# Kernel optimization log

Hardware: AMD Instinct MI355X
Metric: run time of the kernel (lower is better)

## Reference

```python
import jax, jax.numpy as jnp
import numpy as np

TOPK = 9
NUM_CLASSES = 80
IMG = 640
STRIDES = (8, 16, 32)
EPS_IOU = 1e-6   # mmdet BboxOverlaps2D union clamp
EPS_GT = 1e-9    # select_candidates_in_gts eps


def _make_anchors():
    boxes, levels = [], []
    for s in STRIDES:
        n = IMG // s
        c = (np.arange(n, dtype=np.float32) + 0.5) * s
        cx, cy = np.meshgrid(c, c)
        ctr = np.stack([cx.ravel(), cy.ravel()], -1)
        half = 2.5 * s
        boxes.append(np.concatenate([ctr - half, ctr + half], -1))
        levels.append(n * n)
    return np.concatenate(boxes, 0).astype(np.float32), np.array(levels, np.int64)


def setup_inputs() -> dict:
    key = jax.random.key(0)
    ks = jax.random.split(key, 6)
    bs, n_max = 32, 64
    anc, levels = _make_anchors()
    A = anc.shape[0]
    xy = jax.random.uniform(ks[0], (bs, n_max, 2)) * 560.0
    wh = jax.random.uniform(ks[1], (bs, n_max, 2)) * 120.0 + 8.0
    gt_bboxes = jnp.concatenate([xy, xy + wh], -1)
    pxy = jax.random.uniform(ks[2], (bs, A, 2)) * 560.0
    pwh = jax.random.uniform(ks[3], (bs, A, 2)) * 120.0 + 8.0
    pd_bboxes = jnp.concatenate([pxy, pxy + pwh], -1)
    gt_labels = jax.random.randint(ks[4], (bs, n_max, 1), 0, NUM_CLASSES)
    mask_gt = (jax.random.uniform(ks[5], (bs, n_max, 1)) < 0.8).astype(jnp.float32)
    return {"anc_bboxes": jnp.asarray(anc), "n_level_bboxes": levels,
            "gt_labels": gt_labels, "gt_bboxes": gt_bboxes,
            "mask_gt": mask_gt, "pd_bboxes": pd_bboxes}


def _assign(anc_bboxes, levels, gt_labels, gt_bboxes, mask_gt, pd_bboxes):
    A = anc_bboxes.shape[0]
    bs, n_max, _ = gt_bboxes.shape
    gt_flat = gt_bboxes.reshape(-1, 4)
    # pairwise IoU gt vs anchors (mmdet BboxOverlaps2D), (bs, n_max, A)
    lt = jnp.maximum(gt_flat[:, None, :2], anc_bboxes[None, :, :2])
    rb = jnp.minimum(gt_flat[:, None, 2:], anc_bboxes[None, :, 2:])
    inter = jnp.clip(rb - lt, 0).prod(-1)
    area_g = jnp.clip(gt_flat[:, 2:] - gt_flat[:, :2], 0).prod(-1)
    area_a = jnp.clip(anc_bboxes[:, 2:] - anc_bboxes[:, :2], 0).prod(-1)
    union = jnp.maximum(area_g[:, None] + area_a[None, :] - inter, EPS_IOU)
    overlaps = (inter / union).reshape(bs, n_max, A)
    # center distances, (bs, n_max, A)
    gt_c = (gt_flat[:, :2] + gt_flat[:, 2:]) * 0.5
    ac_c = (anc_bboxes[:, :2] + anc_bboxes[:, 2:]) * 0.5
    dist = jnp.sqrt(((gt_c[:, None, :] - ac_c[None, :, :]) ** 2).sum(-1)).reshape(bs, n_max, A)
    # per-level topk (smallest distance) candidates
    mask_gt_b = mask_gt > 0  # (bs, n_max, 1)
    row = jnp.arange(bs * n_max)[:, None]
    is_in_list, idx_list = [], []
    start = 0
    for L in levels:
        k = min(TOPK, L)
        d = dist[..., start:start + L]
        _, idxs = jax.lax.top_k(-d, k)  # (bs, n_max, k)
        idx_list.append(idxs + start)
        idxs_m = jnp.where(mask_gt_b, idxs, 0).reshape(bs * n_max, k)
        cnt = jnp.zeros((bs * n_max, L), dist.dtype).at[row, idxs_m].add(1.0)
        cnt = cnt.reshape(bs, n_max, L)
        is_in_list.append(jnp.where(cnt > 1, jnp.zeros_like(cnt), cnt))
        start += L
    is_in_candidate = jnp.concatenate(is_in_list, -1)  # (bs, n_max, A)
    candidate_idxs = jnp.concatenate(idx_list, -1)     # (bs, n_max, n_levels*k)
    # ATSS threshold = mean + std (unbiased) over candidate overlaps
    cand_ov_full = jnp.where(is_in_candidate > 0, overlaps, jnp.zeros_like(overlaps))
    cand = jnp.take_along_axis(cand_ov_full.reshape(bs * n_max, A),
                               candidate_idxs.reshape(bs * n_max, -1), axis=1)
    cand = cand.reshape(bs, n_max, -1)
    thr = cand.mean(-1, keepdims=True) + cand.std(-1, keepdims=True, ddof=1)
    is_pos = jnp.where(cand_ov_full > thr, is_in_candidate, jnp.zeros_like(is_in_candidate))
    # anchor centers strictly inside gt boxes
    deltas = jnp.concatenate([ac_c[None, None] - gt_bboxes[:, :, None, :2],
                              gt_bboxes[:, :, None, 2:] - ac_c[None, None]], -1)
    is_in_gts = (deltas.min(-1) > EPS_GT).astype(dist.dtype)
    mask_pos = is_pos * is_in_gts * mask_gt  # (bs, n_max, A)
    # resolve anchors assigned to multiple gts by highest IoU (always applied; no-op if no conflicts)
    fg_mask = mask_pos.sum(1)  # (bs, A)
    multi = fg_mask[:, None, :] > 1
    is_max = jnp.transpose(jax.nn.one_hot(overlaps.argmax(1), n_max, dtype=overlaps.dtype), (0, 2, 1))
    mask_pos = jnp.where(multi, is_max, mask_pos)
    fg_mask = mask_pos.sum(1)
    target_gt_idx = mask_pos.argmax(1)  # (bs, A)
    # gather targets
    flat_idx = (target_gt_idx + jnp.arange(bs)[:, None] * n_max).reshape(-1)
    target_labels = gt_labels.reshape(-1)[flat_idx].reshape(bs, A)
    target_labels = jnp.where(fg_mask > 0, target_labels, NUM_CLASSES)
    target_bboxes = gt_flat[flat_idx].reshape(bs, A, 4)
    target_scores = jax.nn.one_hot(target_labels, NUM_CLASSES + 1, dtype=overlaps.dtype)[..., :NUM_CLASSES]
    # scale scores by IoU(gt, pred) of the assigned gt
    lt2 = jnp.maximum(gt_bboxes[:, :, None, :2], pd_bboxes[:, None, :, :2])
    rb2 = jnp.minimum(gt_bboxes[:, :, None, 2:], pd_bboxes[:, None, :, 2:])
    ov2 = jnp.clip(rb2 - lt2, 0).prod(-1)
    a1 = jnp.clip(gt_bboxes[:, :, 2:] - gt_bboxes[:, :, :2], 0).prod(-1)[:, :, None]
    a2 = jnp.clip(pd_bboxes[:, :, 2:] - pd_bboxes[:, :, :2], 0).prod(-1)[:, None, :]
    ious = ov2 / (a1 + a2 - ov2 + 1e-9) * mask_pos
    target_scores = target_scores * jnp.max(ious, axis=1)[..., None]
    return target_labels.astype(jnp.int32), target_bboxes, target_scores, fg_mask > 0


def reference(anc_bboxes, n_level_bboxes, gt_labels, gt_bboxes, mask_gt, pd_bboxes):
    levels = [int(v) for v in np.asarray(n_level_bboxes)]
    return _assign(anc_bboxes, levels, gt_labels, gt_bboxes, mask_gt, pd_bboxes)
```

## Files before the change

### kernel.cpp

```cpp
#include <hip/hip_runtime.h>
#include <stdint.h>

#pragma clang fp contract(off)

#define BS 32
#define NMAX 64
#define A_TOT 8400
#define NC 80

template<int N, int S, int START, int C0>
__device__ __forceinline__ void select_and_iou(
    int ilo, int jlo, float gcx, float gcy,
    float x1, float y1, float x2, float y2, float area_g,
    float* __restrict__ ovrow, int* __restrict__ idxrow)
{
  unsigned long long kk[9];
#pragma unroll
  for (int i = 0; i < 9; ++i) kk[i] = ~0ULL;
  const float s = (float)S;
#pragma unroll
  for (int di = 0; di < 5; ++di) {
    int ii = ilo + di;
    float ay = ((float)ii + 0.5f) * s;
    float dy = gcy - ay;
    float dy2 = dy * dy;
#pragma unroll
    for (int dj = 0; dj < 5; ++dj) {
      int jj = jlo + dj;
      float ax = ((float)jj + 0.5f) * s;
      float dx = gcx - ax;
      float d = sqrtf(dx * dx + dy2);
      unsigned long long key =
          ((unsigned long long)__float_as_uint(d) << 32) |
          (unsigned int)(START + ii * N + jj);
      if (key < kk[8]) {
        kk[8] = key;
#pragma unroll
        for (int t = 8; t > 0; --t) {
          unsigned long long lo = kk[t], hi = kk[t - 1];
          if (lo < hi) { kk[t] = hi; kk[t - 1] = lo; }
        }
      }
    }
  }
#pragma unroll
  for (int t = 0; t < 9; ++t) {
    int aa = (int)(kk[t] & 0xffffffffULL);
    int loc = aa - START;
    int ii = loc / N;
    int jj = loc - ii * N;
    float cx = ((float)jj + 0.5f) * s;
    float cy = ((float)ii + 0.5f) * s;
    const float h = 2.5f * (float)S;
    float ax1 = cx - h, ay1 = cy - h, ax2 = cx + h, ay2 = cy + h;
    float iw = fminf(x2, ax2) - fmaxf(x1, ax1); iw = fmaxf(iw, 0.f);
    float ih = fminf(y2, ay2) - fmaxf(y1, ay1); ih = fmaxf(ih, 0.f);
    float inter = iw * ih;
    float area_a = fmaxf(ax2 - ax1, 0.f) * fmaxf(ay2 - ay1, 0.f);
    float uni = fmaxf(area_g + area_a - inter, 1e-6f);
    ovrow[C0 + t] = inter / uni;
    idxrow[C0 + t] = aa;
  }
}

template<int N, int S, int START, int C0>
__device__ __forceinline__ void scatter_level(
    const float* __restrict__ ovrow, const int* __restrict__ idxrow,
    float thr, float x1, float y1, float x2, float y2,
    int a0, int na, int g, int* s_cnt, int* s_gmin)
{
  const float s = (float)S;
#pragma unroll
  for (int t = 0; t < 9; ++t) {
    float o = ovrow[C0 + t];
    if (o > thr) {
      int aa = idxrow[C0 + t];
      if (aa >= a0 && aa < a0 + na) {
        int loc = aa - START;
        int ii = loc / N;
        int jj = loc - ii * N;
        float cx = ((float)jj + 0.5f) * s;
        float cy = ((float)ii + 0.5f) * s;
        float m = fminf(fminf(cx - x1, cy - y1), fminf(x2 - cx, y2 - cy));
        if (m > 1e-9f) {
          atomicAdd(&s_cnt[aa - a0], 1);
          atomicMin(&s_gmin[aa - a0], g);
        }
      }
    }
  }
}


__global__ __launch_bounds__(256) void atss_fused_k(
    const int* __restrict__ gt_labels,
    const float* __restrict__ gt_bboxes,
    const float* __restrict__ mask_gt,
    const float* __restrict__ pd_bboxes,
    float* __restrict__ out)
{
  __shared__ float s_gt[NMAX * 4];
  __shared__ int   s_lab[NMAX];
  __shared__ float s_ov[NMAX][27];
  __shared__ int   s_idx[NMAX][27];
  __shared__ int   s_cnt[256];
  __shared__ int   s_gmin[256];
  __shared__ int   s_alab[256];
  __shared__ float s_asc[256];

  const int b   = blockIdx.y;
  const int a0  = blockIdx.x * 256;
  const int na  = min(256, A_TOT - a0);
  const int tid = threadIdx.x;

  s_gt[tid] = gt_bboxes[(size_t)b * NMAX * 4 + tid];
  if (tid < NMAX) s_lab[tid] = gt_labels[b * NMAX + tid];
  s_cnt[tid]  = 0;
  s_gmin[tid] = NMAX;
  __syncthreads();

  if (tid < NMAX) {
    const int g = tid;
    if (mask_gt[b * NMAX + g] > 0.0f) {
      float x1 = s_gt[g * 4 + 0], y1 = s_gt[g * 4 + 1];
      float x2 = s_gt[g * 4 + 2], y2 = s_gt[g * 4 + 3];
      float gcx = (x1 + x2) * 0.5f;
      float gcy = (y1 + y2) * 0.5f;

      int jlo0 = min(max((int)floorf(gcx / 8.f)  - 2, 0), 80 - 5);
      int ilo0 = min(max((int)floorf(gcy / 8.f)  - 2, 0), 80 - 5);
      int jlo1 = min(max((int)floorf(gcx / 16.f) - 2, 0), 40 - 5);
      int ilo1 = min(max((int)floorf(gcy / 16.f) - 2, 0), 40 - 5);
      int jlo2 = min(max((int)floorf(gcx / 32.f) - 2, 0), 20 - 5);
      int ilo2 = min(max((int)floorf(gcy / 32.f) - 2, 0), 20 - 5);

      int lo0 = ilo0 * 80 + jlo0,          hi0 = (ilo0 + 4) * 80 + jlo0 + 4;
      int lo1 = 6400 + ilo1 * 40 + jlo1,   hi1 = 6400 + (ilo1 + 4) * 40 + jlo1 + 4;
      int lo2 = 8000 + ilo2 * 20 + jlo2,   hi2 = 8000 + (ilo2 + 4) * 20 + jlo2 + 4;
      bool act = (lo0 < a0 + na && hi0 >= a0) ||
                 (lo1 < a0 + na && hi1 >= a0) ||
                 (lo2 < a0 + na && hi2 >= a0);

      if (act) {
        float area_g = fmaxf(x2 - x1, 0.f) * fmaxf(y2 - y1, 0.f);
        float* ovrow = s_ov[g];
        int*   idxrow = s_idx[g];
        select_and_iou<80,  8,    0,  0>(ilo0, jlo0, gcx, gcy, x1, y1, x2, y2, area_g, ovrow, idxrow);
        select_and_iou<40, 16, 6400,  9>(ilo1, jlo1, gcx, gcy, x1, y1, x2, y2, area_g, ovrow, idxrow);
        select_and_iou<20, 32, 8000, 18>(ilo2, jlo2, gcx, gcy, x1, y1, x2, y2, area_g, ovrow, idxrow);

        float sum = 0.f;
#pragma unroll
        for (int c = 0; c < 27; ++c) sum += ovrow[c];
        float mean = sum / 27.f;
        float ss = 0.f;
#pragma unroll
        for (int c = 0; c < 27; ++c) { float d = ovrow[c] - mean; ss += d * d; }
        float thr = mean + sqrtf(ss / 26.f);

        scatter_level<80,  8,    0,  0>(ovrow, idxrow, thr, x1, y1, x2, y2, a0, na, g, s_cnt, s_gmin);
        scatter_level<40, 16, 6400,  9>(ovrow, idxrow, thr, x1, y1, x2, y2, a0, na, g, s_cnt, s_gmin);
        scatter_level<20, 32, 8000, 18>(ovrow, idxrow, thr, x1, y1, x2, y2, a0, na, g, s_cnt, s_gmin);
      }
    }
  }
  __syncthreads();

  const int a = a0 + tid;
  int lab = NC; float sc = 0.f; int gsel = 0; int fg = 0;

  if (a < A_TOT) {
    const size_t ia = (size_t)b * A_TOT + a;
    const float4 pb = *(const float4*)(pd_bboxes + ia * 4);
    const int c = s_cnt[tid];
    if (c == 1) { gsel = s_gmin[tid]; fg = 1; }
    else if (c > 1) {
      float cx, cy, h;
      if (a < 6400)      { int ii = a / 80;          int jj = a - ii * 80;  cx = ((float)jj + 0.5f) * 8.f;  cy = ((float)ii + 0.5f) * 8.f;  h = 20.f; }
      else if (a < 8000) { int loc = a - 6400; int ii = loc / 40; int jj = loc - ii * 40; cx = ((float)jj + 0.5f) * 16.f; cy = ((float)ii + 0.5f) * 16.f; h = 40.f; }
      else               { int loc = a - 8000; int ii = loc / 20; int jj = loc - ii * 20; cx = ((float)jj + 0.5f) * 32.f; cy = ((float)ii + 0.5f) * 32.f; h = 80.f; }
      float ax1 = cx - h, ay1 = cy - h, ax2 = cx + h, ay2 = cy + h;
      float area_a = fmaxf(ax2 - ax1, 0.f) * fmaxf(ay2 - ay1, 0.f);
      float best = -1.f; int bg = 0;
      for (int gg = 0; gg < NMAX; ++gg) {
        float x1 = s_gt[gg * 4 + 0], y1 = s_gt[gg * 4 + 1];
        float x2 = s_gt[gg * 4 + 2], y2 = s_gt[gg * 4 + 3];
        float iw = fminf(x2, ax2) - fmaxf(x1, ax1); iw = fmaxf(iw, 0.f);
        float ih = fminf(y2, ay2) - fmaxf(y1, ay1); ih = fmaxf(ih, 0.f);
        float inter = iw * ih;
        float ag = fmaxf(x2 - x1, 0.f) * fmaxf(y2 - y1, 0.f);
        float uni = fmaxf(ag + area_a - inter, 1e-6f);
        float iou = inter / uni;
        if (iou > best) { best = iou; bg = gg; }
      }
      gsel = bg; fg = 1;
    }

    if (fg) {
      lab = s_lab[gsel];
      float x1 = s_gt[gsel * 4 + 0], y1 = s_gt[gsel * 4 + 1];
      float x2 = s_gt[gsel * 4 + 2], y2 = s_gt[gsel * 4 + 3];
      float iw = fminf(x2, pb.z) - fmaxf(x1, pb.x); iw = fmaxf(iw, 0.f);
      float ih = fminf(y2, pb.w) - fmaxf(y1, pb.y); ih = fmaxf(ih, 0.f);
      float inter = iw * ih;
      float ag = fmaxf(x2 - x1, 0.f) * fmaxf(y2 - y1, 0.f);
      float ap = fmaxf(pb.z - pb.x, 0.f) * fmaxf(pb.w - pb.y, 0.f);
      sc = inter / (ag + ap - inter + 1e-9f);
    }

    out[ia] = (float)lab;
    float4 bb = { s_gt[gsel * 4 + 0], s_gt[gsel * 4 + 1],
                  s_gt[gsel * 4 + 2], s_gt[gsel * 4 + 3] };
    *(float4*)(out + (size_t)BS * A_TOT + ia * 4) = bb;
    out[(size_t)BS * A_TOT * 85 + ia] = fg ? 1.0f : 0.0f;
  }

  s_alab[tid] = lab;
  s_asc[tid]  = sc;
  __syncthreads();

  float* outS = out + (size_t)BS * A_TOT * 5 + ((size_t)b * A_TOT + a0) * NC;
  const int nv4 = na * (NC / 4);
  for (int i = tid; i < nv4; i += 256) {
    int al = i / (NC / 4);
    int c4 = (i - al * (NC / 4)) * 4;
    int L  = s_alab[al];
    float sv = s_asc[al];
    float4 v;
    v.x = (L == c4 + 0) ? sv : 0.f;
    v.y = (L == c4 + 1) ? sv : 0.f;
    v.z = (L == c4 + 2) ? sv : 0.f;
    v.w = (L == c4 + 3) ? sv : 0.f;
    ((float4*)outS)[i] = v;
  }
}


extern "C" void kernel_launch(void* const* d_in, const int* in_sizes, int n_in,
                              void* d_out, int out_size, void* d_ws, size_t ws_size,
                              hipStream_t stream) {
  const int*   gt_labels = (const int*)  d_in[2];
  const float* gt_bboxes = (const float*)d_in[3];
  const float* mask_gt   = (const float*)d_in[4];
  const float* pd_bboxes = (const float*)d_in[5];
  float* out = (float*)d_out;

  atss_fused_k<<<dim3((A_TOT + 255) / 256, BS), 256, 0, stream>>>(
      gt_labels, gt_bboxes, mask_gt, pd_bboxes, out);
}
```

Before: 136.9 us.

## Split per-GT level top-k across 192 threads and use nontemporal output stores

The serial per-GT candidate selection over three pyramid levels, previously done by 64 threads, is split so that 192 threads each handle one (GT, level) pair. Window bounds and an active flag are staged in shared memory, and two extra barriers separate the phases. Separately, all output writes now use nontemporal stores, so the large score tensor writes stream past the cache. The aim is to shorten the latency-bound selection phase and reduce cache pollution, at the cost of extra synchronisation and shared memory traffic.

```diff
diff --git a/kernel.cpp b/kernel.cpp
--- a/kernel.cpp
+++ b/kernel.cpp
@@ -7,6 +7,8 @@
 #define NMAX 64
 #define A_TOT 8400
 #define NC 80
+
+typedef float vfloat4 __attribute__((ext_vector_type(4)));
 
 template<int N, int S, int START, int C0>
 __device__ __forceinline__ void select_and_iou(
@@ -107,6 +109,9 @@
   __shared__ int   s_gmin[256];
   __shared__ int   s_alab[256];
   __shared__ float s_asc[256];
+  __shared__ short s_ilo[3][NMAX];
+  __shared__ short s_jlo[3][NMAX];
+  __shared__ unsigned char s_act[NMAX];
 
   const int b   = blockIdx.y;
   const int a0  = blockIdx.x * 256;
@@ -121,6 +126,7 @@
 
   if (tid < NMAX) {
     const int g = tid;
+    bool act = false;
     if (mask_gt[b * NMAX + g] > 0.0f) {
       float x1 = s_gt[g * 4 + 0], y1 = s_gt[g * 4 + 1];
       float x2 = s_gt[g * 4 + 2], y2 = s_gt[g * 4 + 3];
@@ -133,36 +139,62 @@
       int ilo1 = min(max((int)floorf(gcy / 16.f) - 2, 0), 40 - 5);
       int jlo2 = min(max((int)floorf(gcx / 32.f) - 2, 0), 20 - 5);
       int ilo2 = min(max((int)floorf(gcy / 32.f) - 2, 0), 20 - 5);
+      s_jlo[0][g] = (short)jlo0; s_ilo[0][g] = (short)ilo0;
+      s_jlo[1][g] = (short)jlo1; s_ilo[1][g] = (short)ilo1;
+      s_jlo[2][g] = (short)jlo2; s_ilo[2][g] = (short)ilo2;
 
       int lo0 = ilo0 * 80 + jlo0,          hi0 = (ilo0 + 4) * 80 + jlo0 + 4;
       int lo1 = 6400 + ilo1 * 40 + jlo1,   hi1 = 6400 + (ilo1 + 4) * 40 + jlo1 + 4;
       int lo2 = 8000 + ilo2 * 20 + jlo2,   hi2 = 8000 + (ilo2 + 4) * 20 + jlo2 + 4;
-      bool act = (lo0 < a0 + na && hi0 >= a0) ||
-                 (lo1 < a0 + na && hi1 >= a0) ||
-                 (lo2 < a0 + na && hi2 >= a0);
-
-      if (act) {
-        float area_g = fmaxf(x2 - x1, 0.f) * fmaxf(y2 - y1, 0.f);
-        float* ovrow = s_ov[g];
-        int*   idxrow = s_idx[g];
-        select_and_iou<80,  8,    0,  0>(ilo0, jlo0, gcx, gcy, x1, y1, x2, y2, area_g, ovrow, idxrow);
-        select_and_iou<40, 16, 6400,  9>(ilo1, jlo1, gcx, gcy, x1, y1, x2, y2, area_g, ovrow, idxrow);
-        select_and_iou<20, 32, 8000, 18>(ilo2, jlo2, gcx, gcy, x1, y1, x2, y2, area_g, ovrow, idxrow);
-
-        float sum = 0.f;
-#pragma unroll
-        for (int c = 0; c < 27; ++c) sum += ovrow[c];
-        float mean = sum / 27.f;
-        float ss = 0.f;
-#pragma unroll
-        for (int c = 0; c < 27; ++c) { float d = ovrow[c] - mean; ss += d * d; }
-        float thr = mean + sqrtf(ss / 26.f);
-
-        scatter_level<80,  8,    0,  0>(ovrow, idxrow, thr, x1, y1, x2, y2, a0, na, g, s_cnt, s_gmin);
-        scatter_level<40, 16, 6400,  9>(ovrow, idxrow, thr, x1, y1, x2, y2, a0, na, g, s_cnt, s_gmin);
-        scatter_level<20, 32, 8000, 18>(ovrow, idxrow, thr, x1, y1, x2, y2, a0, na, g, s_cnt, s_gmin);
-      }
-    }
+      act = (lo0 < a0 + na && hi0 >= a0) ||
+            (lo1 < a0 + na && hi1 >= a0) ||
+            (lo2 < a0 + na && hi2 >= a0);
+    }
+    s_act[tid] = act ? 1 : 0;
+  }
+  __syncthreads();
+
+  if (tid < 192) {
+    const int g  = tid & 63;
+    const int lv = tid >> 6;
+    if (s_act[g]) {
+      float x1 = s_gt[g * 4 + 0], y1 = s_gt[g * 4 + 1];
+      float x2 = s_gt[g * 4 + 2], y2 = s_gt[g * 4 + 3];
+      float gcx = (x1 + x2) * 0.5f;
+      float gcy = (y1 + y2) * 0.5f;
+      float area_g = fmaxf(x2 - x1, 0.f) * fmaxf(y2 - y1, 0.f);
+      float* ovrow  = s_ov[g];
+      int*   idxrow = s_idx[g];
+      int ilo = s_ilo[lv][g], jlo = s_jlo[lv][g];
+      if (lv == 0)
+        select_and_iou<80,  8,    0,  0>(ilo, jlo, gcx, gcy, x1, y1, x2, y2, area_g, ovrow, idxrow);
+      else if (lv == 1)
+        select_and_iou<40, 16, 6400,  9>(ilo, jlo, gcx, gcy, x1, y1, x2, y2, area_g, ovrow, idxrow);
+      else
+        select_and_iou<20, 32, 8000, 18>(ilo, jlo, gcx, gcy, x1, y1, x2, y2, area_g, ovrow, idxrow);
+    }
+  }
+  __syncthreads();
+
+  if (tid < NMAX && s_act[tid]) {
+    const int g = tid;
+    float x1 = s_gt[g * 4 + 0], y1 = s_gt[g * 4 + 1];
+    float x2 = s_gt[g * 4 + 2], y2 = s_gt[g * 4 + 3];
+    const float* ovrow  = s_ov[g];
+    const int*   idxrow = s_idx[g];
+
+    float sum = 0.f;
+#pragma unroll
+    for (int c = 0; c < 27; ++c) sum += ovrow[c];
+    float mean = sum / 27.f;
+    float ss = 0.f;
+#pragma unroll
+    for (int c = 0; c < 27; ++c) { float d = ovrow[c] - mean; ss += d * d; }
+    float thr = mean + sqrtf(ss / 26.f);
+
+    scatter_level<80,  8,    0,  0>(ovrow, idxrow, thr, x1, y1, x2, y2, a0, na, g, s_cnt, s_gmin);
+    scatter_level<40, 16, 6400,  9>(ovrow, idxrow, thr, x1, y1, x2, y2, a0, na, g, s_cnt, s_gmin);
+    scatter_level<20, 32, 8000, 18>(ovrow, idxrow, thr, x1, y1, x2, y2, a0, na, g, s_cnt, s_gmin);
   }
   __syncthreads();
 
@@ -208,11 +240,11 @@
       sc = inter / (ag + ap - inter + 1e-9f);
     }
 
-    out[ia] = (float)lab;
-    float4 bb = { s_gt[gsel * 4 + 0], s_gt[gsel * 4 + 1],
-                  s_gt[gsel * 4 + 2], s_gt[gsel * 4 + 3] };
-    *(float4*)(out + (size_t)BS * A_TOT + ia * 4) = bb;
-    out[(size_t)BS * A_TOT * 85 + ia] = fg ? 1.0f : 0.0f;
+    __builtin_nontemporal_store((float)lab, out + ia);
+    vfloat4 bb = { s_gt[gsel * 4 + 0], s_gt[gsel * 4 + 1],
+                   s_gt[gsel * 4 + 2], s_gt[gsel * 4 + 3] };
+    __builtin_nontemporal_store(bb, (vfloat4*)(out + (size_t)BS * A_TOT + ia * 4));
+    __builtin_nontemporal_store(fg ? 1.0f : 0.0f, out + (size_t)BS * A_TOT * 85 + ia);
   }
 
   s_alab[tid] = lab;
@@ -226,12 +258,12 @@
     int c4 = (i - al * (NC / 4)) * 4;
     int L  = s_alab[al];
     float sv = s_asc[al];
-    float4 v;
+    vfloat4 v;
     v.x = (L == c4 + 0) ? sv : 0.f;
     v.y = (L == c4 + 1) ? sv : 0.f;
     v.z = (L == c4 + 2) ? sv : 0.f;
     v.w = (L == c4 + 3) ? sv : 0.f;
-    ((float4*)outS)[i] = v;
+    __builtin_nontemporal_store(v, ((vfloat4*)outS) + i);
   }
 }
 
```

Result: faster. 127.9 us (-6.6%).
